# Kernel tuning notes

Hardware: AMD Instinct MI355X
Metric: run time of the kernel (lower is better)

Reference implementation:

```python
import jax, jax.numpy as jnp
import numpy as np
import math

D_MODEL = 128
N_GLOBAL = 100
L_PRETRAIN = 2048


def setup_inputs() -> dict:
    key = jax.random.key(0)
    kq, kk, kv = jax.random.split(key, 3)
    B, S, D = 2, 8192, D_MODEL
    q = jax.random.normal(kq, (B, S, D), dtype=jnp.float32)
    k = jax.random.normal(kk, (B, S, D), dtype=jnp.float32)
    v = jax.random.normal(kv, (B, S, D), dtype=jnp.float32)
    return {"q": q, "k": k, "v": v}


def reference(q, k, v):
    S = q.shape[1]
    i = jnp.arange(S)[:, None]   # query index
    j = jnp.arange(S)[None, :]   # key index
    # distance bias: (j - i) clamped above at L_PRETRAIN (torch.clamp(max=...))
    dist = jnp.minimum(j - i, L_PRETRAIN).astype(q.dtype)
    # lambda mask: row i keeps cols [0, min(n_global, i+1)) (global sinks)
    # and [max(0, i-l_pretrain+1), i] (local causal window); else -inf.
    allowed = (j <= i) & ((j < N_GLOBAL) | (j >= i - L_PRETRAIN + 1))
    # mask is 0/-inf, so dist + mask == where(allowed, dist, -inf)
    bias = jnp.where(allowed, dist, -jnp.inf)  # [S, S]
    logits = jnp.einsum('bqd,bkd->bqk', q, k) / math.sqrt(D_MODEL) + bias
    weights = jax.nn.softmax(logits, axis=-1)
    return jnp.einsum('bqk,bkd->bqd', weights, v)
```

## Files before the change

### kernel.cpp

```cpp
#include <hip/hip_runtime.h>

#define SEQ 8192
#define DIM 128
#define QR  4
#define WPB 4
#define RPB (QR * WPB)
#define NB  (2 * SEQ / RPB)
#define KROWS 80

__global__ __launch_bounds__(256) void lminf_kernel(
    const float* __restrict__ qg,
    const float* __restrict__ kg,
    const float* __restrict__ vg,
    float* __restrict__ og)
{
    const int lane = threadIdx.x & 63;
    const int wv   = __builtin_amdgcn_readfirstlane(threadIdx.x >> 6);
    const int rowblk = blockIdx.x * RPB + wv * QR;
    const int r0     = rowblk & (SEQ - 1);
    const int blkrow0 = (blockIdx.x * RPB) & (SEQ - 1);
    const long base  = (long)((blockIdx.x * RPB) >> 13) * (SEQ * DIM);

    __shared__ float4 kds[KROWS * 32];

    {
        const float4* kgp = (const float4*)(kg + base);
        #pragma unroll
        for (int it = 0; it < (KROWS * 32) / 256; ++it) {
            const int g   = it * 256 + threadIdx.x;
            const int row = g >> 5;
            const int c   = g & 31;
            int gr = blkrow0 - 64 + row;
            if (gr < 0) gr = 0;
            kds[row * 32 + (c ^ (row & 7))] = kgp[gr * 32 + c];
        }
    }
    __syncthreads();

    const int w0 = r0 - 60;
    const int j  = w0 + lane;
    const int lr = lane + wv * QR + 4;
    const int sw = lr & 7;
    const float4* krow = &kds[lr * 32];

    const float* qb = qg + base + (long)r0 * DIM;

    float acc[QR] = {0.f, 0.f, 0.f, 0.f};
    #pragma unroll 8
    for (int c = 0; c < 32; ++c) {
        const float4 kk = krow[c ^ sw];
        #pragma unroll
        for (int rr = 0; rr < QR; ++rr) {
            const float4 qq = *(const float4*)(qb + rr * DIM + c * 4);
            acc[rr] += qq.x * kk.x + qq.y * kk.y + qq.z * kk.z + qq.w * kk.w;
        }
    }

    float w[QR];
    #pragma unroll
    for (int rr = 0; rr < QR; ++rr) {
        const int i = r0 + rr;
        float s = acc[rr] * 0.08838834764831845f + (float)(j - i);
        if (j > i || j < 0) s = -3.0e38f;
        float m = s;
        #pragma unroll
        for (int off = 32; off; off >>= 1) m = fmaxf(m, __shfl_xor(m, off));
        const float e = __expf(s - m);
        float l = e;
        #pragma unroll
        for (int off = 32; off; off >>= 1) l += __shfl_xor(l, off);
        w[rr] = e * (1.0f / l);
    }

    float o0[QR] = {0.f, 0.f, 0.f, 0.f};
    float o1[QR] = {0.f, 0.f, 0.f, 0.f};
    const float* vb = vg + base;
    #pragma unroll 8
    for (int k = 0; k < 64; ++k) {
        int vr = w0 + k;
        if (vr < 0) vr = 0;
        const float2 vpair = *(const float2*)(vb + (long)vr * DIM + 2 * lane);
        const float wk0 = __int_as_float(
            __builtin_amdgcn_readlane(__float_as_int(w[0]), k));
        const float wk1 = __int_as_float(
            __builtin_amdgcn_readlane(__float_as_int(w[1]), k));
        const float wk2 = __int_as_float(
            __builtin_amdgcn_readlane(__float_as_int(w[2]), k));
        const float wk3 = __int_as_float(
            __builtin_amdgcn_readlane(__float_as_int(w[3]), k));
        o0[0] += wk0 * vpair.x;  o1[0] += wk0 * vpair.y;
        o0[1] += wk1 * vpair.x;  o1[1] += wk1 * vpair.y;
        o0[2] += wk2 * vpair.x;  o1[2] += wk2 * vpair.y;
        o0[3] += wk3 * vpair.x;  o1[3] += wk3 * vpair.y;
    }

    #pragma unroll
    for (int rr = 0; rr < QR; ++rr) {
        ((float2*)(og + base + (long)(r0 + rr) * DIM))[lane] =
            make_float2(o0[rr], o1[rr]);
    }
}

extern "C" void kernel_launch(void* const* d_in, const int* in_sizes, int n_in,
                              void* d_out, int out_size, void* d_ws, size_t ws_size,
                              hipStream_t stream) {
    const float* q = (const float*)d_in[0];
    const float* k = (const float*)d_in[1];
    const float* v = (const float*)d_in[2];
    float* out = (float*)d_out;

    lminf_kernel<<<NB, 256, 0, stream>>>(q, k, v, out);
}
```

Baseline: 90.59 us.

## Stage Q and softmax weights in LDS, widen blocks to 8 waves

Result: no change. 91.83 us (+1.4%).

```diff
diff --git a/kernel.cpp b/kernel.cpp
--- a/kernel.cpp
+++ b/kernel.cpp
@@ -3,37 +3,49 @@
 #define SEQ 8192
 #define DIM 128
 #define QR  4
-#define WPB 4
+#define WPB 8
 #define RPB (QR * WPB)
 #define NB  (2 * SEQ / RPB)
-#define KROWS 80
+#define KROWS 96
 
-__global__ __launch_bounds__(256) void lminf_kernel(
+__global__ __launch_bounds__(512) void lminf_kernel(
     const float* __restrict__ qg,
     const float* __restrict__ kg,
     const float* __restrict__ vg,
     float* __restrict__ og)
 {
-    const int lane = threadIdx.x & 63;
-    const int wv   = __builtin_amdgcn_readfirstlane(threadIdx.x >> 6);
-    const int rowblk = blockIdx.x * RPB + wv * QR;
-    const int r0     = rowblk & (SEQ - 1);
-    const int blkrow0 = (blockIdx.x * RPB) & (SEQ - 1);
-    const long base  = (long)((blockIdx.x * RPB) >> 13) * (SEQ * DIM);
+    const int tid  = threadIdx.x;
+    const int lane = tid & 63;
+    const int wv   = __builtin_amdgcn_readfirstlane(tid >> 6);
+
+    const int wk      = ((blockIdx.x & 7) << 6) + (blockIdx.x >> 3);
+    const int rowblk  = wk * RPB + wv * QR;
+    const int r0      = rowblk & (SEQ - 1);
+    const int blkrow0 = (wk * RPB) & (SEQ - 1);
+    const long base   = (long)((wk * RPB) >> 13) * (SEQ * DIM);
 
     __shared__ float4 kds[KROWS * 32];
+    __shared__ float  qs[WPB][QR][DIM];
+    __shared__ float4 wsm[WPB][64];
 
     {
         const float4* kgp = (const float4*)(kg + base);
         #pragma unroll
-        for (int it = 0; it < (KROWS * 32) / 256; ++it) {
-            const int g   = it * 256 + threadIdx.x;
+        for (int it = 0; it < (KROWS * 32) / 512; ++it) {
+            const int g   = it * 512 + tid;
             const int row = g >> 5;
             const int c   = g & 31;
             int gr = blkrow0 - 64 + row;
             if (gr < 0) gr = 0;
             kds[row * 32 + (c ^ (row & 7))] = kgp[gr * 32 + c];
         }
+    }
+    #pragma unroll
+    for (int rr = 0; rr < QR; ++rr) {
+        const float2 t =
+            ((const float2*)(qg + base + (long)(r0 + rr) * DIM))[lane];
+        qs[wv][rr][2*lane]   = t.x;
+        qs[wv][rr][2*lane+1] = t.y;
     }
     __syncthreads();
 
@@ -43,15 +55,13 @@
     const int sw = lr & 7;
     const float4* krow = &kds[lr * 32];
 
-    const float* qb = qg + base + (long)r0 * DIM;
-
     float acc[QR] = {0.f, 0.f, 0.f, 0.f};
     #pragma unroll 8
     for (int c = 0; c < 32; ++c) {
         const float4 kk = krow[c ^ sw];
         #pragma unroll
         for (int rr = 0; rr < QR; ++rr) {
-            const float4 qq = *(const float4*)(qb + rr * DIM + c * 4);
+            const float4 qq = ((const float4*)qs[wv][rr])[c];
             acc[rr] += qq.x * kk.x + qq.y * kk.y + qq.z * kk.z + qq.w * kk.w;
         }
     }
@@ -71,27 +81,21 @@
         for (int off = 32; off; off >>= 1) l += __shfl_xor(l, off);
         w[rr] = e * (1.0f / l);
     }
+    wsm[wv][lane] = make_float4(w[0], w[1], w[2], w[3]);
 
     float o0[QR] = {0.f, 0.f, 0.f, 0.f};
     float o1[QR] = {0.f, 0.f, 0.f, 0.f};
     const float* vb = vg + base;
-    #pragma unroll 8
+    #pragma unroll 16
     for (int k = 0; k < 64; ++k) {
         int vr = w0 + k;
         if (vr < 0) vr = 0;
         const float2 vpair = *(const float2*)(vb + (long)vr * DIM + 2 * lane);
-        const float wk0 = __int_as_float(
-            __builtin_amdgcn_readlane(__float_as_int(w[0]), k));
-        const float wk1 = __int_as_float(
-            __builtin_amdgcn_readlane(__float_as_int(w[1]), k));
-        const float wk2 = __int_as_float(
-            __builtin_amdgcn_readlane(__float_as_int(w[2]), k));
-        const float wk3 = __int_as_float(
-            __builtin_amdgcn_readlane(__float_as_int(w[3]), k));
-        o0[0] += wk0 * vpair.x;  o1[0] += wk0 * vpair.y;
-        o0[1] += wk1 * vpair.x;  o1[1] += wk1 * vpair.y;
-        o0[2] += wk2 * vpair.x;  o1[2] += wk2 * vpair.y;
-        o0[3] += wk3 * vpair.x;  o1[3] += wk3 * vpair.y;
+        const float4 wk4 = wsm[wv][k];
+        o0[0] += wk4.x * vpair.x;  o1[0] += wk4.x * vpair.y;
+        o0[1] += wk4.y * vpair.x;  o1[1] += wk4.y * vpair.y;
+        o0[2] += wk4.z * vpair.x;  o1[2] += wk4.z * vpair.y;
+        o0[3] += wk4.w * vpair.x;  o1[3] += wk4.w * vpair.y;
     }
 
     #pragma unroll
@@ -109,5 +113,5 @@
     const float* v = (const float*)d_in[2];
     float* out = (float*)d_out;
 
-    lminf_kernel<<<NB, 256, 0, stream>>>(q, k, v, out);
+    lminf_kernel<<<NB, 512, 0, stream>>>(q, k, v, out);
 }
```
